# Optimization experiments

Measured on AMD Instinct MI355X. Metric: run time of the kernel, lower is better.

Reference implementation:

```python
import jax, jax.numpy as jnp
import numpy as np

B, CS, CT, H, W = 16, 512, 512, 64, 64

def setup_inputs() -> dict:
    key = jax.random.key(0)
    k1, k2 = jax.random.split(key)
    x = jax.random.normal(k1, (B, CS, H, W), dtype=jnp.float32)
    # 16 Linear weights, each [out_ch, in_ch] (torch Linear layout), stacked
    Wg = jax.random.normal(k2, (16, CT, CS), dtype=jnp.float32) * (2.0 / CT) ** 0.5
    return {"x": x, "Wg": Wg}

def reference(x, Wg):
    # x: [B, Cs, H, W]; Wg: [16, Ct, Cs] indexed by phase r*4+c, r=(i%4), c=(j%4)
    # Dropout is identity in eval mode (deterministic reference).
    b, cs, h, w = x.shape
    ct = Wg.shape[1]
    Wrq = Wg.reshape(4, 4, ct, cs)               # [r, q, Ct, Cs]
    xr = x.reshape(b, cs, h // 4, 4, w // 4, 4)  # [b, c, h4, r, w4, q]
    # grouped matmul: each (r,q) phase uses its own weight
    out = jnp.einsum('bchrwq,rqoc->bohrwq', xr, Wrq)
    return out.reshape(b, ct, h, w)
```

## Files before the change

### kernel.cpp

```cpp
#include <hip/hip_runtime.h>
#include <stdint.h>


typedef __attribute__((ext_vector_type(8))) short short8;
typedef __attribute__((ext_vector_type(4))) float f32x4;

#define CS 512
#define CT 512
#define HW 4096
#define BK 32
#define MT 128
#define NR 8
#define BPITCH 40

__device__ __forceinline__ uint16_t f32_to_bf16(float f) {
    uint32_t u = __builtin_bit_cast(uint32_t, f);
    u += 0x7FFFu + ((u >> 16) & 1u);
    return (uint16_t)(u >> 16);
}

__global__ __launch_bounds__(256)
void w2_cvt(const float* __restrict__ Wg, uint16_t* __restrict__ W2) {
    int idx = (blockIdx.x * 256 + threadIdx.x) * 8;
    float4 a = *(const float4*)(Wg + idx);
    float4 b = *(const float4*)(Wg + idx + 4);
    uint16_t o[8];
    o[0]=f32_to_bf16(a.x); o[1]=f32_to_bf16(a.y); o[2]=f32_to_bf16(a.z); o[3]=f32_to_bf16(a.w);
    o[4]=f32_to_bf16(b.x); o[5]=f32_to_bf16(b.y); o[6]=f32_to_bf16(b.z); o[7]=f32_to_bf16(b.w);
    *(short8*)(W2 + idx) = *(short8*)o;
}

template<bool USE_W2>
__global__ __launch_bounds__(512, 2)
void gwl_main(const float* __restrict__ x, const float* __restrict__ Wg,
              const uint16_t* __restrict__ W2, float* __restrict__ out) {
    const int nb = blockIdx.x;
    const int mb = blockIdx.y;
    const int r  = blockIdx.z;
    const int m0 = mb * MT;

    __shared__ __align__(16) unsigned char smem[73728];
    uint16_t* As = (uint16_t*)smem;
    uint16_t* Bs = (uint16_t*)(smem + 32768);
    float*    T  = (float*)smem;

    const int tid  = threadIdx.x;
    const int lane = tid & 63;
    const int wave = tid >> 6;
    const int q    = wave & 3;
    const int mw   = wave >> 2;
    const int lr = lane & 15, qd = lane >> 4;

    const int w16 = tid & 15;
    const int rho = (tid >> 4) & 7;
    const int kw  = tid >> 7;
    const int rg  = nb * NR + rho;
    const int bb  = rg >> 4;
    const int h4  = rg & 15;
    const float* bbase = x + (size_t)bb * CS * HW
                           + (size_t)((h4 * 4 + r) * 64 + w16 * 4);

    const uint16_t* abase = USE_W2
        ? W2 + ((size_t)(r * 4 + q) * CT + m0 + mw * 64) * CS : (const uint16_t*)nullptr;

    float4 breg[8];
    auto loadB = [&](int k0) {
        const float* p = bbase + (size_t)(k0 + kw * 8) * HW;
        #pragma unroll
        for (int cc = 0; cc < 8; ++cc) breg[cc] = *(const float4*)(p + (size_t)cc * HW);
    };
    auto writeB = [&]() {
        #pragma unroll
        for (int qq = 0; qq < 4; ++qq) {
            uint16_t tmp[8];
            #pragma unroll
            for (int cc = 0; cc < 8; ++cc)
                tmp[cc] = f32_to_bf16(((const float*)&breg[cc])[qq]);
            *(short8*)(Bs + (qq * 128 + rho * 16 + w16) * BPITCH + kw * 8) = *(short8*)tmp;
        }
    };
    auto stageA_glds = [&](int k0) {
        #pragma unroll
        for (int t = 0; t < 4; ++t) {
            const uint16_t* src = abase + (size_t)(t * 16 + (lane >> 2)) * CS
                                        + k0 + (((lane & 3) ^ ((lane >> 2) & 3)) * 8);
            uint16_t* dst = As + (q * 128 + mw * 64) * 32 + t * 512;
            __builtin_amdgcn_global_load_lds(
                (const __attribute__((address_space(1))) void*)src,
                (__attribute__((address_space(3))) void*)dst, 16, 0, 0);
        }
    };
    auto stageA_fp32 = [&](int k0) {
        const int qa = tid >> 7, rem = tid & 127;
        const int ka = rem & 7, ma = rem >> 3;
        const float* ap = Wg + ((size_t)(r * 4 + qa) * CT + m0 + ma) * CS + k0 + ka * 4;
        const int kc = (((ka >> 1) ^ (ma & 3)) * 8) + (ka & 1) * 4;
        #pragma unroll
        for (int it = 0; it < 8; ++it) {
            float4 v = *(const float4*)(ap + (size_t)it * 16 * CS);
            uint16_t tmp[4] = {f32_to_bf16(v.x), f32_to_bf16(v.y),
                               f32_to_bf16(v.z), f32_to_bf16(v.w)};
            *(uint64_t*)(As + (qa * 128 + ma + it * 16) * 32 + kc) =
                *(const uint64_t*)tmp;
        }
    };

    f32x4 acc[4][8] = {};

    loadB(0);
    if (USE_W2) stageA_glds(0); else stageA_fp32(0);
    writeB();
    loadB(BK);

    const uint16_t* Asq = As + (q * 128 + mw * 64) * 32;
    const uint16_t* Bsq = Bs + q * 128 * BPITCH;

    for (int k = 0; k < 16; ++k) {
        __syncthreads();
        short8 afr[4], bfr[8];
        #pragma unroll
        for (int i = 0; i < 4; ++i)
            afr[i] = *(const short8*)(Asq + (i * 16 + lr) * 32 + ((qd ^ (lr & 3)) * 8));
        #pragma unroll
        for (int j = 0; j < 8; ++j)
            bfr[j] = *(const short8*)(Bsq + (j * 16 + lr) * BPITCH + qd * 8);
        if (k < 15) {
            __syncthreads();
            if (USE_W2) stageA_glds((k + 1) * BK); else stageA_fp32((k + 1) * BK);
            writeB();
            if (k < 14) loadB((k + 2) * BK);
        }
        #pragma unroll
        for (int i = 0; i < 4; ++i)
            #pragma unroll
            for (int j = 0; j < 8; ++j)
                acc[i][j] = __builtin_amdgcn_mfma_f32_16x16x32_bf16(
                    afr[i], bfr[j], acc[i][j], 0, 0, 0);
    }

    const int m16s = tid >> 5;
    const int rs   = (tid >> 2) & 7;
    const int ws   = (tid & 3) * 16;
    const int rgs  = nb * NR + rs;
    const int obb  = rgs >> 4;
    const int oh4  = rgs & 15;
    #pragma unroll
    for (int ic = 0; ic < 8; ++ic) {
        __syncthreads();
        if (mw == (ic >> 2)) {
            const int i = ic & 3;
            #pragma unroll
            for (int j = 0; j < 8; ++j)
                #pragma unroll
                for (int g = 0; g < 4; ++g)
                    T[((qd * 4 + g) * 8 + j) * 68 + lr * 4 + q] = acc[i][j][g];
        }
        __syncthreads();
        float* op = out + ((size_t)obb * CT + m0 + ic * 16 + m16s) * HW
                        + (oh4 * 4 + r) * 64 + ws;
        const float* tp = T + (m16s * 8 + rs) * 68 + ws;
        #pragma unroll
        for (int c = 0; c < 4; ++c)
            ((float4*)op)[c] = ((const float4*)tp)[c];
    }
}

extern "C" void kernel_launch(void* const* d_in, const int* in_sizes, int n_in,
                              void* d_out, int out_size, void* d_ws, size_t ws_size,
                              hipStream_t stream) {
    const float* x  = (const float*)d_in[0];
    const float* Wg = (const float*)d_in[1];
    float* out = (float*)d_out;
    dim3 grid(32, 4, 4);
    if (ws_size >= (size_t)16 * 512 * 512 * 2) {
        uint16_t* W2 = (uint16_t*)d_ws;
        w2_cvt<<<2048, 256, 0, stream>>>(Wg, W2);
        gwl_main<true><<<grid, 512, 0, stream>>>(x, Wg, W2, out);
    } else {
        gwl_main<false><<<grid, 512, 0, stream>>>(x, Wg, nullptr, out);
    }
}
```

Baseline: 314.5 us.

## Double-buffer LDS tiles with one barrier per k-step and revised swizzle

Shared memory is split into two ping-pong buffers. Each k-iteration stages the next A/B tile into the alternate buffer while issuing MFMAs on the current one, which drops one of the two __syncthreads per step. It adds explicit vmcnt/lgkmcnt waits, a single s_barrier and a sched_barrier to order loads and LDS writes. The A-tile XOR swizzle now uses row bits 1-2 instead of 0-1 to change the LDS bank pattern. LDS per block doubles to 144 KB, so only one 512-thread block fits per CU instead of two, which may cost the latency hiding the extra blocks provided.

```diff
diff --git a/kernel.cpp b/kernel.cpp
--- a/kernel.cpp
+++ b/kernel.cpp
@@ -12,6 +12,7 @@
 #define MT 128
 #define NR 8
 #define BPITCH 40
+#define BUFB 73728
 
 __device__ __forceinline__ uint16_t f32_to_bf16(float f) {
     uint32_t u = __builtin_bit_cast(uint32_t, f);
@@ -39,10 +40,8 @@
     const int r  = blockIdx.z;
     const int m0 = mb * MT;
 
-    __shared__ __align__(16) unsigned char smem[73728];
-    uint16_t* As = (uint16_t*)smem;
-    uint16_t* Bs = (uint16_t*)(smem + 32768);
-    float*    T  = (float*)smem;
+    __shared__ __align__(16) unsigned char smem[2 * BUFB];
+    float* T = (float*)smem;
 
     const int tid  = threadIdx.x;
     const int lane = tid & 63;
@@ -69,73 +68,90 @@
         #pragma unroll
         for (int cc = 0; cc < 8; ++cc) breg[cc] = *(const float4*)(p + (size_t)cc * HW);
     };
-    auto writeB = [&]() {
+    auto writeB = [&](uint16_t* BsD) {
         #pragma unroll
         for (int qq = 0; qq < 4; ++qq) {
             uint16_t tmp[8];
             #pragma unroll
             for (int cc = 0; cc < 8; ++cc)
                 tmp[cc] = f32_to_bf16(((const float*)&breg[cc])[qq]);
-            *(short8*)(Bs + (qq * 128 + rho * 16 + w16) * BPITCH + kw * 8) = *(short8*)tmp;
+            *(short8*)(BsD + (qq * 128 + rho * 16 + w16) * BPITCH + kw * 8) = *(short8*)tmp;
         }
     };
-    auto stageA_glds = [&](int k0) {
+    auto stageA_glds = [&](int k0, uint16_t* AsD) {
         #pragma unroll
         for (int t = 0; t < 4; ++t) {
             const uint16_t* src = abase + (size_t)(t * 16 + (lane >> 2)) * CS
-                                        + k0 + (((lane & 3) ^ ((lane >> 2) & 3)) * 8);
-            uint16_t* dst = As + (q * 128 + mw * 64) * 32 + t * 512;
+                                        + k0 + (((lane & 3) ^ ((lane >> 3) & 3)) * 8);
+            uint16_t* dst = AsD + (q * 128 + mw * 64) * 32 + t * 512;
             __builtin_amdgcn_global_load_lds(
                 (const __attribute__((address_space(1))) void*)src,
                 (__attribute__((address_space(3))) void*)dst, 16, 0, 0);
         }
     };
-    auto stageA_fp32 = [&](int k0) {
+    auto stageA_fp32 = [&](int k0, uint16_t* AsD) {
         const int qa = tid >> 7, rem = tid & 127;
         const int ka = rem & 7, ma = rem >> 3;
         const float* ap = Wg + ((size_t)(r * 4 + qa) * CT + m0 + ma) * CS + k0 + ka * 4;
-        const int kc = (((ka >> 1) ^ (ma & 3)) * 8) + (ka & 1) * 4;
+        const int kc = (((ka >> 1) ^ ((ma >> 1) & 3)) * 8) + (ka & 1) * 4;
         #pragma unroll
         for (int it = 0; it < 8; ++it) {
             float4 v = *(const float4*)(ap + (size_t)it * 16 * CS);
             uint16_t tmp[4] = {f32_to_bf16(v.x), f32_to_bf16(v.y),
                                f32_to_bf16(v.z), f32_to_bf16(v.w)};
-            *(uint64_t*)(As + (qa * 128 + ma + it * 16) * 32 + kc) =
+            *(uint64_t*)(AsD + (qa * 128 + ma + it * 16) * 32 + kc) =
                 *(const uint64_t*)tmp;
         }
     };
 
     f32x4 acc[4][8] = {};
 
-    loadB(0);
-    if (USE_W2) stageA_glds(0); else stageA_fp32(0);
-    writeB();
-    loadB(BK);
-
-    const uint16_t* Asq = As + (q * 128 + mw * 64) * 32;
-    const uint16_t* Bsq = Bs + q * 128 * BPITCH;
+    {
+        uint16_t* As0 = (uint16_t*)smem;
+        uint16_t* Bs0 = (uint16_t*)(smem + 32768);
+        loadB(0);
+        if (USE_W2) stageA_glds(0, As0); else stageA_fp32(0, As0);
+        writeB(Bs0);
+        loadB(BK);
+        __syncthreads();
+    }
 
     for (int k = 0; k < 16; ++k) {
-        __syncthreads();
+        const uint16_t* Asq = (const uint16_t*)(smem + (k & 1) * BUFB)
+                              + (q * 128 + mw * 64) * 32;
+        const uint16_t* Bsq = (const uint16_t*)(smem + (k & 1) * BUFB + 32768)
+                              + q * 128 * BPITCH;
         short8 afr[4], bfr[8];
         #pragma unroll
         for (int i = 0; i < 4; ++i)
-            afr[i] = *(const short8*)(Asq + (i * 16 + lr) * 32 + ((qd ^ (lr & 3)) * 8));
+            afr[i] = *(const short8*)(Asq + (i * 16 + lr) * 32
+                                      + ((qd ^ ((lr >> 1) & 3)) * 8));
         #pragma unroll
         for (int j = 0; j < 8; ++j)
             bfr[j] = *(const short8*)(Bsq + (j * 16 + lr) * BPITCH + qd * 8);
+
         if (k < 15) {
-            __syncthreads();
-            if (USE_W2) stageA_glds((k + 1) * BK); else stageA_fp32((k + 1) * BK);
-            writeB();
+            uint16_t* AsN = (uint16_t*)(smem + ((k + 1) & 1) * BUFB);
+            uint16_t* BsN = (uint16_t*)(smem + ((k + 1) & 1) * BUFB + 32768);
+            if (USE_W2) stageA_glds((k + 1) * BK, AsN); else stageA_fp32((k + 1) * BK, AsN);
+            __builtin_amdgcn_sched_barrier(0x38F);
+            writeB(BsN);
             if (k < 14) loadB((k + 2) * BK);
         }
+
         #pragma unroll
         for (int i = 0; i < 4; ++i)
             #pragma unroll
             for (int j = 0; j < 8; ++j)
                 acc[i][j] = __builtin_amdgcn_mfma_f32_16x16x32_bf16(
                     afr[i], bfr[j], acc[i][j], 0, 0, 0);
+
+        if (k < 15) {
+            if (k < 14) asm volatile("s_waitcnt vmcnt(8)" ::: "memory");
+            else        asm volatile("s_waitcnt vmcnt(0)" ::: "memory");
+            asm volatile("s_waitcnt lgkmcnt(0)" ::: "memory");
+            __builtin_amdgcn_s_barrier();
+        }
     }
 
     const int m16s = tid >> 5;
```

Result: faster. 298.4 us (-5.1%).
